# Performance work log

Measured on AMD Instinct MI355X. Metric: run time of the kernel, lower is better.

The kernel has to match this reference:

```python
import jax, jax.numpy as jnp
import numpy as np
from jax import lax

REG_STRENGTH = 0.01
TEMPERATURE = 0.1


def _pav_nonincreasing(y):
    """Pool-adjacent-violators for isotonic L2 regression with a
    nonincreasing constraint (matches torchsort's isotonic_l2).
    Returns (solution [n], block_id [n])."""
    n = y.shape[0]

    def body(carry, yi):
        m, c, t = carry  # block means, block counts, stack top
        m = m.at[t].set(yi)
        c = c.at[t].set(1)

        def cond(st):
            m_, c_, t_ = st
            return (t_ > 0) & (m_[t_ - 1] < m_[t_])

        def merge(st):
            m_, c_, t_ = st
            tot = m_[t_ - 1] * c_[t_ - 1] + m_[t_] * c_[t_]
            cc = c_[t_ - 1] + c_[t_]
            m_ = m_.at[t_ - 1].set(tot / cc)
            c_ = c_.at[t_ - 1].set(cc).at[t_].set(0)
            return (m_, c_, t_ - 1)

        m, c, t = lax.while_loop(cond, merge, (m, c, t))
        return (m, c, t + 1), None

    init = (jnp.zeros(n, y.dtype), jnp.zeros(n, jnp.int32), jnp.int32(0))
    (m, c, _), _ = lax.scan(body, init, y)
    sol = jnp.repeat(m, c, total_repeat_length=n)
    blk = jnp.repeat(jnp.arange(n), c, total_repeat_length=n)
    return sol, blk


@jax.custom_vjp
def _isotonic_l2(y):
    return _pav_nonincreasing(y)[0]


def _iso_fwd(y):
    sol, blk = _pav_nonincreasing(y)
    return sol, blk


def _iso_bwd(blk, g):
    n = g.shape[0]
    sums = jax.ops.segment_sum(g, blk, num_segments=n)
    cnts = jax.ops.segment_sum(jnp.ones_like(g), blk, num_segments=n)
    return ((sums / jnp.maximum(cnts, 1.0))[blk],)


_isotonic_l2.defvjp(_iso_fwd, _iso_bwd)


def soft_sort_ascending(scores, reg_strength):
    """torchsort.soft_sort with L2 regularization. scores: [B, R]."""
    n = scores.shape[-1]
    w = jnp.arange(n, 0, -1, dtype=scores.dtype) / reg_strength  # [n, ..., 1]/rs
    perm = jnp.argsort(scores, axis=-1)
    s = -jnp.take_along_axis(scores, perm, axis=-1)  # descending sort of -scores
    sol = jax.vmap(_isotonic_l2)(w[None, :] - s)
    return sol - w  # ascending soft-sorted values, [B, R]


def setup_inputs() -> dict:
    key = jax.random.key(0)
    k1, k2 = jax.random.split(key)
    scores = jax.random.normal(k1, (128, 8192), dtype=jnp.float32)
    ref_class = jax.random.randint(k2, (8192,), 0, 10, dtype=jnp.int32)
    return {"scores": scores, "ref_class": ref_class, "k": 32, "K": 8}


def reference(scores, ref_class, k, K):
    B, R = scores.shape
    rc = ref_class
    if rc.ndim == 1:
        rc = jnp.broadcast_to(rc[None, :], (B, R))
    rc = rc.astype(scores.dtype)
    sorted_vals = soft_sort_ascending(scores, REG_STRENGTH)  # [B, R]
    yk = sorted_vals[:, -k:]                                  # top-k largest, [B, k]
    M = jnp.abs(scores[:, None, :] - yk[:, :, None])          # [B, k, R]
    soft_mask = jax.nn.softmax(-M / TEMPERATURE, axis=-1)     # [B, k, R]
    soft_label_expectation = jnp.einsum('bkr,br->bk', soft_mask, rc)
    return yk, soft_label_expectation
```

## Files before the change

### kernel.cpp

```cpp
#include <hip/hip_runtime.h>
#include <math.h>

#define R_N    8192
#define K_TOP  32
#define HALF_R 4096
#define CAND   512
#define C1     14.426950408889634f
#define NEG_BIG (-3.0e38f)

__device__ __forceinline__ float fast_exp2(float x) {
#if __has_builtin(__builtin_amdgcn_exp2f)
    return __builtin_amdgcn_exp2f(x);
#else
    return exp2f(x);
#endif
}

__device__ __forceinline__ float merge_asc32(float v, int l) {
#pragma unroll
    for (int j = 16; j > 0; j >>= 1) {
        float pv = __shfl_xor(v, j, 64);
        v = ((l & j) == 0) ? fminf(v, pv) : fmaxf(v, pv);
    }
    return v;
}

__device__ __forceinline__ float sort32_asc(float v, int l) {
#pragma unroll
    for (int k = 2; k <= 32; k <<= 1) {
#pragma unroll
        for (int j = k >> 1; j > 0; j >>= 1) {
            float pv = __shfl_xor(v, j, 64);
            bool keep_min = (((l & k) == 0) == ((l & j) == 0));
            v = keep_min ? fminf(v, pv) : fmaxf(v, pv);
        }
    }
    return v;
}

__device__ __forceinline__ float sort64_asc(float v, int lane) {
#pragma unroll
    for (int k = 2; k <= 64; k <<= 1) {
#pragma unroll
        for (int j = k >> 1; j > 0; j >>= 1) {
            float pv = __shfl_xor(v, j, 64);
            bool keep_min = (((lane & k) == 0) == ((lane & j) == 0));
            v = keep_min ? fminf(v, pv) : fmaxf(v, pv);
        }
    }
    return v;
}

__device__ __forceinline__ float merge_top32(float a, float b, int l) {
    float rev = __shfl_xor(b, 31, 64);
    return merge_asc32(fmaxf(a, rev), l);
}

extern "C" __global__ void __launch_bounds__(512)
k_topk(const float* __restrict__ scores, float* __restrict__ wstop) {
    __shared__ float    cand[CAND];
    __shared__ float    twbuf[8];
    __shared__ unsigned cnt;
    __shared__ float    topbuf[16 * 32];

    const int row  = blockIdx.x >> 1;
    const int half = blockIdx.x & 1;
    const int tid  = threadIdx.x;
    const int lane = tid & 63;
    const int l    = tid & 31;
    const int h    = tid >> 5;
    const int wv   = tid >> 6;

    const float4* s4 = (const float4*)(scores + (size_t)row * R_N + half * HALF_R);
    float4 a = s4[tid];
    float4 b = s4[tid + 512];
    float v[8] = {a.x, a.y, a.z, a.w, b.x, b.y, b.z, b.w};

    cand[tid] = NEG_BIG;
    if (tid == 0) cnt = 0;

    float tmax = v[0];
#pragma unroll
    for (int e = 1; e < 8; ++e) tmax = fmaxf(tmax, v[e]);
    float srt = sort64_asc(tmax, lane);
    float t_w = __shfl(srt, 32, 64);
    if (lane == 0) twbuf[wv] = t_w;
    __syncthreads();
    float t = twbuf[0];
#pragma unroll
    for (int w = 1; w < 8; ++w) t = fmaxf(t, twbuf[w]);

    unsigned long long m[8];
    unsigned tot = 0;
#pragma unroll
    for (int e = 0; e < 8; ++e) {
        m[e] = __ballot(v[e] >= t);
        tot += (unsigned)__popcll(m[e]);
    }
    unsigned wbase = 0;
    if (lane == 0) wbase = atomicAdd(&cnt, tot);
    wbase = __shfl(wbase, 0, 64);
    const unsigned long long lt = (1ull << lane) - 1ull;
#pragma unroll
    for (int e = 0; e < 8; ++e) {
        if (v[e] >= t) {
            unsigned idx = wbase + (unsigned)__popcll(m[e] & lt);
            if (idx < CAND) cand[idx] = v[e];
        }
        wbase += (unsigned)__popcll(m[e]);
    }
    __syncthreads();

    float run = sort32_asc(cand[tid], l);
#pragma unroll
    for (int stride = 1; stride < 16; stride <<= 1) {
        topbuf[h * 32 + l] = run;
        __syncthreads();
        if ((h & (2 * stride - 1)) == 0) {
            float pv = topbuf[(h + stride) * 32 + (l ^ 31)];
            run = merge_asc32(fmaxf(run, pv), l);
        }
        __syncthreads();
    }
    if (tid < 32) wstop[(size_t)blockIdx.x * K_TOP + l] = run;
}

extern "C" __global__ void __launch_bounds__(1024)
k_expect(const float* __restrict__ scores, const int* __restrict__ rc,
         const float* __restrict__ wstop, float* __restrict__ out, int B) {
    __shared__ float    dsS[32], dsC[32];
    __shared__ unsigned dcnt;
    __shared__ float    pbuf[16 * 2];

    const int row  = blockIdx.x;
    const int tid  = threadIdx.x;
    const int lane = tid & 63;
    const int l    = tid & 31;
    const int wv   = tid >> 6;

    if (tid == 0) dcnt = 0;

    float A  = wstop[(size_t)row * 2 * K_TOP + l];
    float Bv = wstop[(size_t)row * 2 * K_TOP + K_TOP + l];
    float yk = merge_top32(A, Bv, l);
    if (tid < 32) out[(size_t)row * K_TOP + l] = yk;
    const float y0 = __shfl(yk, 0, 64);

    const float4* s4 = (const float4*)(scores + (size_t)row * R_N);
    const int4*   c4 = (const int4*)rc;
    float4 sa = s4[tid], sb = s4[tid + 1024];
    int4   ca = c4[tid], cb = c4[tid + 1024];
    float se[8] = {sa.x, sa.y, sa.z, sa.w, sb.x, sb.y, sb.z, sb.w};
    float ce[8] = {(float)ca.x, (float)ca.y, (float)ca.z, (float)ca.w,
                   (float)cb.x, (float)cb.y, (float)cb.z, (float)cb.w};
    __syncthreads();

    float P = 0.f, Pc = 0.f;
#pragma unroll
    for (int e = 0; e < 8; ++e) {
        if (se[e] <= y0) {
            float ex = fast_exp2(C1 * se[e]);
            P += ex;
            Pc = fmaf(ce[e], ex, Pc);
        } else {
            unsigned idx = atomicAdd(&dcnt, 1u);
            dsS[idx] = se[e];
            dsC[idx] = ce[e];
        }
    }
#pragma unroll
    for (int off = 32; off > 0; off >>= 1) {
        P  += __shfl_xor(P,  off, 64);
        Pc += __shfl_xor(Pc, off, 64);
    }
    if (lane == 0) { pbuf[wv * 2] = P; pbuf[wv * 2 + 1] = Pc; }
    __syncthreads();
    float Pt = 0.f, Pct = 0.f;
#pragma unroll
    for (int w = 0; w < 16; ++w) { Pt += pbuf[w * 2]; Pct += pbuf[w * 2 + 1]; }
    const int nD = (int)dcnt;

    const float yj0 = __shfl(yk, 2 * wv,     64);
    const float yj1 = __shfl(yk, 2 * wv + 1, 64);
    float n0 = 0.f, d0 = 0.f, n1 = 0.f, d1 = 0.f;
    if (lane < nD) {
        float s = dsS[lane], c = dsC[lane];
        float e0 = fast_exp2(-C1 * fabsf(s - yj0));
        float e1 = fast_exp2(-C1 * fabsf(s - yj1));
        d0 = e0; n0 = c * e0;
        d1 = e1; n1 = c * e1;
    }
#pragma unroll
    for (int off = 32; off > 0; off >>= 1) {
        n0 += __shfl_xor(n0, off, 64); d0 += __shfl_xor(d0, off, 64);
        n1 += __shfl_xor(n1, off, 64); d1 += __shfl_xor(d1, off, 64);
    }
    if (lane == 0) {
        float e0 = fast_exp2(-C1 * yj0);
        float e1 = fast_exp2(-C1 * yj1);
        float* dst = out + (size_t)B * K_TOP + (size_t)row * K_TOP + 2 * wv;
        dst[0] = fmaf(Pct, e0, n0) / fmaf(Pt, e0, d0);
        dst[1] = fmaf(Pct, e1, n1) / fmaf(Pt, e1, d1);
    }
}

extern "C" void kernel_launch(void* const* d_in, const int* in_sizes, int n_in,
                              void* d_out, int out_size, void* d_ws, size_t ws_size,
                              hipStream_t stream) {
    const float* scores = (const float*)d_in[0];
    const int*   rc     = (const int*)d_in[1];
    const int R = in_sizes[1];
    const int B = in_sizes[0] / R;
    float* out   = (float*)d_out;
    float* wstop = (float*)d_ws;

    hipLaunchKernelGGL(k_topk,   dim3(B * 2), dim3(512),  0, stream, scores, wstop);
    hipLaunchKernelGGL(k_expect, dim3(B),     dim3(1024), 0, stream, scores, rc, wstop, out, B);
}
```

Baseline: 68.32 us.

## Fuse top-k selection and soft-mask expectation into one per-row kernel

Merges the two-kernel pipeline (half-row top-k partials, then merge plus expectation) into a single 1024-thread block per row that loads the row once, finds the top 32 through threshold filtering and a bitonic merge tree, and then computes the softmax expectations. This removes a second launch, the workspace round-trip, and the reload of scores. The trade-off is that the top-k phase now uses only 128 blocks instead of 256, and the merge tree gains one more synchronized level.

```diff
diff --git a/kernel.cpp b/kernel.cpp
--- a/kernel.cpp
+++ b/kernel.cpp
@@ -3,8 +3,7 @@
 
 #define R_N    8192
 #define K_TOP  32
-#define HALF_R 4096
-#define CAND   512
+#define CAND   1024
 #define C1     14.426950408889634f
 #define NEG_BIG (-3.0e38f)
 
@@ -51,61 +50,62 @@
     return v;
 }
 
-__device__ __forceinline__ float merge_top32(float a, float b, int l) {
-    float rev = __shfl_xor(b, 31, 64);
-    return merge_asc32(fmaxf(a, rev), l);
-}
+extern "C" __global__ void __launch_bounds__(1024)
+k_fused(const float* __restrict__ scores, const int* __restrict__ rc,
+        float* __restrict__ out, int B) {
+    __shared__ float    cand[CAND];
+    __shared__ float    topbuf[32 * 32];
+    __shared__ float    twbuf[16];
+    __shared__ float    yk_lds[K_TOP];
+    __shared__ float    pbuf[16 * 2];
+    __shared__ float    dsS[32], dsC[32];
+    __shared__ unsigned cnt, dcnt;
 
-extern "C" __global__ void __launch_bounds__(512)
-k_topk(const float* __restrict__ scores, float* __restrict__ wstop) {
-    __shared__ float    cand[CAND];
-    __shared__ float    twbuf[8];
-    __shared__ unsigned cnt;
-    __shared__ float    topbuf[16 * 32];
-
-    const int row  = blockIdx.x >> 1;
-    const int half = blockIdx.x & 1;
+    const int row  = blockIdx.x;
     const int tid  = threadIdx.x;
     const int lane = tid & 63;
     const int l    = tid & 31;
     const int h    = tid >> 5;
     const int wv   = tid >> 6;
 
-    const float4* s4 = (const float4*)(scores + (size_t)row * R_N + half * HALF_R);
-    float4 a = s4[tid];
-    float4 b = s4[tid + 512];
-    float v[8] = {a.x, a.y, a.z, a.w, b.x, b.y, b.z, b.w};
+    const float4* s4 = (const float4*)(scores + (size_t)row * R_N);
+    const int4*   c4 = (const int4*)rc;
+    float4 sa = s4[tid], sb = s4[tid + 1024];
+    int4   ca = c4[tid], cb = c4[tid + 1024];
+    float se[8] = {sa.x, sa.y, sa.z, sa.w, sb.x, sb.y, sb.z, sb.w};
+    float ce[8] = {(float)ca.x, (float)ca.y, (float)ca.z, (float)ca.w,
+                   (float)cb.x, (float)cb.y, (float)cb.z, (float)cb.w};
 
-    cand[tid] = NEG_BIG;
-    if (tid == 0) cnt = 0;
+    cand[tid & (CAND - 1)] = NEG_BIG;
+    if (tid == 0) { cnt = 0; dcnt = 0; }
 
-    float tmax = v[0];
+    float tmax = se[0];
 #pragma unroll
-    for (int e = 1; e < 8; ++e) tmax = fmaxf(tmax, v[e]);
+    for (int e = 1; e < 8; ++e) tmax = fmaxf(tmax, se[e]);
     float srt = sort64_asc(tmax, lane);
     float t_w = __shfl(srt, 32, 64);
     if (lane == 0) twbuf[wv] = t_w;
     __syncthreads();
     float t = twbuf[0];
 #pragma unroll
-    for (int w = 1; w < 8; ++w) t = fmaxf(t, twbuf[w]);
+    for (int w = 1; w < 16; ++w) t = fmaxf(t, twbuf[w]);
 
     unsigned long long m[8];
     unsigned tot = 0;
 #pragma unroll
     for (int e = 0; e < 8; ++e) {
-        m[e] = __ballot(v[e] >= t);
+        m[e] = __ballot(se[e] >= t);
         tot += (unsigned)__popcll(m[e]);
     }
     unsigned wbase = 0;
     if (lane == 0) wbase = atomicAdd(&cnt, tot);
     wbase = __shfl(wbase, 0, 64);
-    const unsigned long long lt = (1ull << lane) - 1ull;
+    const unsigned long long ltm = (1ull << lane) - 1ull;
 #pragma unroll
     for (int e = 0; e < 8; ++e) {
-        if (v[e] >= t) {
-            unsigned idx = wbase + (unsigned)__popcll(m[e] & lt);
-            if (idx < CAND) cand[idx] = v[e];
+        if (se[e] >= t) {
+            unsigned idx = wbase + (unsigned)__popcll(m[e] & ltm);
+            if (idx < CAND) cand[idx] = se[e];
         }
         wbase += (unsigned)__popcll(m[e]);
     }
@@ -113,7 +113,7 @@
 
     float run = sort32_asc(cand[tid], l);
 #pragma unroll
-    for (int stride = 1; stride < 16; stride <<= 1) {
+    for (int stride = 1; stride < 32; stride <<= 1) {
         topbuf[h * 32 + l] = run;
         __syncthreads();
         if ((h & (2 * stride - 1)) == 0) {
@@ -122,38 +122,12 @@
         }
         __syncthreads();
     }
-    if (tid < 32) wstop[(size_t)blockIdx.x * K_TOP + l] = run;
-}
-
-extern "C" __global__ void __launch_bounds__(1024)
-k_expect(const float* __restrict__ scores, const int* __restrict__ rc,
-         const float* __restrict__ wstop, float* __restrict__ out, int B) {
-    __shared__ float    dsS[32], dsC[32];
-    __shared__ unsigned dcnt;
-    __shared__ float    pbuf[16 * 2];
-
-    const int row  = blockIdx.x;
-    const int tid  = threadIdx.x;
-    const int lane = tid & 63;
-    const int l    = tid & 31;
-    const int wv   = tid >> 6;
-
-    if (tid == 0) dcnt = 0;
-
-    float A  = wstop[(size_t)row * 2 * K_TOP + l];
-    float Bv = wstop[(size_t)row * 2 * K_TOP + K_TOP + l];
-    float yk = merge_top32(A, Bv, l);
-    if (tid < 32) out[(size_t)row * K_TOP + l] = yk;
-    const float y0 = __shfl(yk, 0, 64);
-
-    const float4* s4 = (const float4*)(scores + (size_t)row * R_N);
-    const int4*   c4 = (const int4*)rc;
-    float4 sa = s4[tid], sb = s4[tid + 1024];
-    int4   ca = c4[tid], cb = c4[tid + 1024];
-    float se[8] = {sa.x, sa.y, sa.z, sa.w, sb.x, sb.y, sb.z, sb.w};
-    float ce[8] = {(float)ca.x, (float)ca.y, (float)ca.z, (float)ca.w,
-                   (float)cb.x, (float)cb.y, (float)cb.z, (float)cb.w};
+    if (tid < 32) {
+        yk_lds[l] = run;
+        out[(size_t)row * K_TOP + l] = run;
+    }
     __syncthreads();
+    const float y0 = yk_lds[0];
 
     float P = 0.f, Pc = 0.f;
 #pragma unroll
@@ -180,8 +154,8 @@
     for (int w = 0; w < 16; ++w) { Pt += pbuf[w * 2]; Pct += pbuf[w * 2 + 1]; }
     const int nD = (int)dcnt;
 
-    const float yj0 = __shfl(yk, 2 * wv,     64);
-    const float yj1 = __shfl(yk, 2 * wv + 1, 64);
+    const float yj0 = yk_lds[2 * wv];
+    const float yj1 = yk_lds[2 * wv + 1];
     float n0 = 0.f, d0 = 0.f, n1 = 0.f, d1 = 0.f;
     if (lane < nD) {
         float s = dsS[lane], c = dsC[lane];
@@ -211,9 +185,7 @@
     const int*   rc     = (const int*)d_in[1];
     const int R = in_sizes[1];
     const int B = in_sizes[0] / R;
-    float* out   = (float*)d_out;
-    float* wstop = (float*)d_ws;
+    float* out = (float*)d_out;
 
-    hipLaunchKernelGGL(k_topk,   dim3(B * 2), dim3(512),  0, stream, scores, wstop);
-    hipLaunchKernelGGL(k_expect, dim3(B),     dim3(1024), 0, stream, scores, rc, wstop, out, B);
+    hipLaunchKernelGGL(k_fused, dim3(B), dim3(1024), 0, stream, scores, rc, out, B);
 }
```

After: 66.59 us (median of 2 runs). -2.5%, faster.
